# Performance work log

Hardware: AMD Instinct MI355X
Metric: run time of the kernel (lower is better)

Reference implementation:

```python
import jax, jax.numpy as jnp
import numpy as np

BETA = 0.25

def setup_inputs() -> dict:
    key = jax.random.key(0)
    k1, k2 = jax.random.split(key)
    z_e = jax.random.normal(k1, (32, 256, 32, 32), dtype=jnp.float32)
    embed_weight = jax.random.normal(k2, (4096, 256), dtype=jnp.float32) * 0.1
    return {"z_e": z_e, "embed_weight": embed_weight}

def reference(z_e, embed_weight):
    # Eval-mode forward (no input noise, no EMA buffer update).
    B, C, H, W = z_e.shape
    K = embed_weight.shape[0]
    z_t = jnp.transpose(z_e, (0, 2, 3, 1))            # [B,H,W,C]
    z_flat = z_t.reshape(-1, C)                        # [N,C]
    # Squared Euclidean distances; argmin is identical to argmin of cdist(p=2).
    d = (
        jnp.sum(z_flat * z_flat, axis=1, keepdims=True)
        - 2.0 * (z_flat @ embed_weight.T)
        + jnp.sum(embed_weight * embed_weight, axis=1)
    )                                                  # [N,K]
    idx = jnp.argmin(d, axis=1)                        # [N]
    # utilization = (#unique codes used) / vocab_size, jit-safe via bincount-style scatter
    counts = jnp.zeros((K,), dtype=jnp.float32).at[idx].add(1.0)
    utilization = jnp.sum(counts > 0).astype(jnp.float32) / K
    z_q = embed_weight[idx].reshape(B, H, W, C)        # [B,H,W,C]
    commitment_loss = jnp.mean((jax.lax.stop_gradient(z_q) - z_t) ** 2) * BETA
    z_q_st = z_t + jax.lax.stop_gradient(z_q - z_t)    # straight-through
    return jnp.transpose(z_q_st, (0, 3, 1, 2)), commitment_loss, utilization
```

## Files before the change

### kernel.cpp

```cpp
#include <hip/hip_runtime.h>
#include <math.h>


#define W 0.05f

using half8 = __attribute__((ext_vector_type(8))) _Float16;
using f32x4 = __attribute__((ext_vector_type(4))) float;

__device__ __forceinline__ void gload_lds16(const void* g, void* l) {
  __builtin_amdgcn_global_load_lds(
      (const __attribute__((address_space(1))) unsigned int*)g,
      (__attribute__((address_space(3))) unsigned int*)l, 16, 0, 0);
}

__device__ __forceinline__ bool lexlt(float v, int x, float ov, int ox) {
  return (v < ov) || (v == ov && x < ox);
}
__device__ __forceinline__ bool lexlt64(double v, int x, double ov, int ox) {
  return (v < ov) || (v == ov && x < ox);
}

__device__ __forceinline__ void ins3(float d, int c,
                                     float& a0, float& a1, float& a2,
                                     int& b0, int& b1, int& b2) {
  const bool l0 = d < a0, l1 = d < a1, l2 = d < a2;
  a2 = l1 ? a1 : (l2 ? d : a2);
  b2 = l1 ? b1 : (l2 ? c : b2);
  a1 = l0 ? a0 : (l1 ? d : a1);
  b1 = l0 ? b0 : (l1 ? c : b1);
  a0 = l0 ? d : a0;
  b0 = l0 ? c : b0;
}

__device__ __forceinline__ void mrg3(float& a0, float& a1, float& a2,
                                     int& x0, int& x1, int& x2,
                                     float b0, float b1, float b2,
                                     int y0, int y1, int y2) {
  const bool A = lexlt(a0, x0, b0, y0);
  const float w0 = A ? a0 : b0; const int w0x = A ? x0 : y0;
  const float fw = A ? a1 : b1; const int fwx = A ? x1 : y1;
  const float ls = A ? b0 : a0; const int lsx = A ? y0 : x0;
  const bool B = lexlt(fw, fwx, ls, lsx);
  const float w1 = B ? fw : ls; const int w1x = B ? fwx : lsx;
  const float t1 = A ? a2 : b2; const int t1x = A ? x2 : y2;
  const float l2v = A ? b1 : a1; const int l2x = A ? y1 : x1;
  const float c1 = B ? t1 : fw; const int c1x = B ? t1x : fwx;
  const float c2 = B ? ls : l2v; const int c2x = B ? lsx : l2x;
  const bool C = lexlt(c1, c1x, c2, c2x);
  a0 = w0; x0 = w0x; a1 = w1; x1 = w1x;
  a2 = C ? c1 : c2; x2 = C ? c1x : c2x;
}

__global__ __launch_bounds__(256) void vq_prep(const float* __restrict__ E,
                                               uint4* __restrict__ Epk,
                                               float* __restrict__ enorm) {
  const int t = blockIdx.x * 256 + threadIdx.x;
  const int code = t >> 5, jj = t & 31;
  const int slice = jj >> 3, j = jj & 7;
  const int cg = code >> 7, c = code & 127;
  const float* src = E + (size_t)code * 256 + jj * 8;
  union { half8 h; uint4 u; } pk;
  float s = 0.f;
#pragma unroll
  for (int e = 0; e < 8; ++e) {
    const float z = src[e];
    s = fmaf(z, z, s);
    pk.h[e] = (_Float16)(z * 256.0f);
  }
  const size_t g = (size_t)((cg * 4 + slice) * 1024) + c * 8 + (j ^ (c & 7));
  Epk[g] = pk.u;
#pragma unroll
  for (int off = 1; off < 32; off <<= 1) s += __shfl_xor(s, off);
  if (jj == 0) enorm[code] = s;
}

__global__ __launch_bounds__(256, 2) void vq_screen(
    const float* __restrict__ Z, const char* __restrict__ Epk,
    const float* __restrict__ enorm,
    float* __restrict__ pv0, float* __restrict__ pv1, float* __restrict__ pv2,
    int* __restrict__ pi0, int* __restrict__ pi1, int* __restrict__ pi2) {
  __shared__ char lds[65536];
  const int tid = threadIdx.x;
  const int w = tid >> 6, l = tid & 63;
  const int qg = blockIdx.x >> 1, half = blockIdx.x & 1;
  const int qbase = qg * 128;
  const int b = qbase >> 10;
  const int hwq = (qbase & 1023) + w * 32 + (l & 15);

  const float* Zq = Z + (size_t)b * 262144 + hwq;
  half8 ah[2][8];
#pragma unroll
  for (int u = 0; u < 2; ++u)
#pragma unroll
    for (int ks = 0; ks < 8; ++ks) {
      const int c0 = ks * 32 + (l >> 4) * 8;
#pragma unroll
      for (int e = 0; e < 8; ++e)
        ah[u][ks][e] = (_Float16)(Zq[u * 16 + ((size_t)(c0 + e) << 10)] * 256.0f);
    }

  int lo[4];
#pragma unroll
  for (int s = 0; s < 4; ++s)
    lo[s] = (s >> 1) * 16384 + (l & 15) * 128 +
            ((((s & 1) * 4 + (l >> 4)) ^ (l & 7)) << 4);

  float m0[2][4], m1[2][4], m2[2][4];
  int x0[2][4], x1[2][4], x2[2][4];
#pragma unroll
  for (int u = 0; u < 2; ++u)
#pragma unroll
    for (int r = 0; r < 4; ++r) {
      m0[u][r] = INFINITY; m1[u][r] = INFINITY; m2[u][r] = INFINITY;
      x0[u][r] = 0x7fffffff; x1[u][r] = 0x7fffffff; x2[u][r] = 0x7fffffff;
    }

  const int sbase = half * 32;
  auto stage = [&](int sel, int ss) {
    const char* src = Epk + ((size_t)(sbase + ss) << 15) + w * 8192 + l * 16;
    char* dst = lds + sel * 32768 + w * 8192;
#pragma unroll
    for (int i = 0; i < 8; ++i) gload_lds16(src + i * 1024, dst + i * 1024);
  };
  stage(0, 0);

  for (int chunk = 0; chunk < 16; ++chunk) {
    f32x4 acc[2][8];
#pragma unroll
    for (int u = 0; u < 2; ++u)
#pragma unroll
      for (int t = 0; t < 8; ++t) acc[u][t] = (f32x4){0.f, 0.f, 0.f, 0.f};

    for (int h = 0; h < 2; ++h) {
      const int ss = chunk * 2 + h;
      __syncthreads();
      if (ss + 1 < 32) stage((ss + 1) & 1, ss + 1);
      const char* Lb = lds + (ss & 1) * 32768;
      __builtin_amdgcn_s_setprio(1);
#pragma unroll
      for (int s = 0; s < 4; ++s) {
        const int ksg = h * 4 + s;
#pragma unroll
        for (int t = 0; t < 8; ++t) {
          const half8 eh = *(const half8*)(Lb + t * 2048 + lo[s]);
          acc[0][t] = __builtin_amdgcn_mfma_f32_16x16x32_f16(ah[0][ksg], eh, acc[0][t], 0, 0, 0);
          acc[1][t] = __builtin_amdgcn_mfma_f32_16x16x32_f16(ah[1][ksg], eh, acc[1][t], 0, 0, 0);
        }
      }
      __builtin_amdgcn_s_setprio(0);
    }

    const int cb = half * 2048 + chunk * 128;
#pragma unroll
    for (int t = 0; t < 8; ++t) {
      const int code = cb + t * 16 + (l & 15);
      const float en = enorm[code];
#pragma unroll
      for (int u = 0; u < 2; ++u)
#pragma unroll
        for (int r = 0; r < 4; ++r) {
          const float d = fmaf(acc[u][t][r], -3.0517578125e-05f, en);
          ins3(d, code, m0[u][r], m1[u][r], m2[u][r], x0[u][r], x1[u][r], x2[u][r]);
        }
    }
  }

#pragma unroll
  for (int mask = 1; mask <= 8; mask <<= 1) {
#pragma unroll
    for (int u = 0; u < 2; ++u)
#pragma unroll
      for (int r = 0; r < 4; ++r) {
        const float o0 = __shfl_xor(m0[u][r], mask);
        const float o1 = __shfl_xor(m1[u][r], mask);
        const float o2 = __shfl_xor(m2[u][r], mask);
        const int y0 = __shfl_xor(x0[u][r], mask);
        const int y1 = __shfl_xor(x1[u][r], mask);
        const int y2 = __shfl_xor(x2[u][r], mask);
        mrg3(m0[u][r], m1[u][r], m2[u][r], x0[u][r], x1[u][r], x2[u][r],
             o0, o1, o2, y0, y1, y2);
      }
  }
  if ((l & 15) == 0) {
#pragma unroll
    for (int u = 0; u < 2; ++u)
#pragma unroll
      for (int r = 0; r < 4; ++r) {
        const int n = qbase + w * 32 + u * 16 + (l >> 4) * 4 + r;
        const int o = half * 32768 + n;
        pv0[o] = m0[u][r]; pv1[o] = m1[u][r]; pv2[o] = m2[u][r];
        pi0[o] = x0[u][r]; pi1[o] = x1[u][r]; pi2[o] = x2[u][r];
      }
  }
}

__global__ __launch_bounds__(256) void vq_merge(
    float* __restrict__ pv0, float* __restrict__ pv1, float* __restrict__ pv2,
    int* __restrict__ pi0, int* __restrict__ pi1, int* __restrict__ pi2,
    int* __restrict__ idxOut, int* __restrict__ cand, int* __restrict__ candCount,
    int* __restrict__ messy, int* __restrict__ messyCount) {
  const int n = blockIdx.x * 256 + threadIdx.x;
  float a0 = pv0[n], a1 = pv1[n], a2 = pv2[n];
  int x0 = pi0[n], x1 = pi1[n], x2 = pi2[n];
  mrg3(a0, a1, a2, x0, x1, x2,
       pv0[n + 32768], pv1[n + 32768], pv2[n + 32768],
       pi0[n + 32768], pi1[n + 32768], pi2[n + 32768]);
  idxOut[n] = x0;
  pi0[n] = x0; pi1[n] = x1; pi2[n] = x2;
  if (a1 - a0 < W) {
    if (a2 - a0 < W) {
      const int p = atomicAdd(messyCount, 1);
      if (p < 2048) messy[p] = n;
    } else {
      const int p = atomicAdd(candCount, 1);
      cand[p] = n;
    }
  }
}

__global__ __launch_bounds__(256) void vq_cand3(
    const float* __restrict__ Z, const float* __restrict__ E,
    const int* __restrict__ pi0, const int* __restrict__ pi1,
    const int* __restrict__ pi2, const int* __restrict__ cand,
    const int* __restrict__ candCount, int* __restrict__ idxOut) {
  const int w = threadIdx.x >> 6, l = threadIdx.x & 63;
  const int cnt = *candCount;
  for (int j = blockIdx.x * 4 + w; j < cnt; j += gridDim.x * 4) {
    const int n = cand[j];
    const int b = n >> 10, hw = n & 1023;
    const int ca = pi0[n], cbn = pi1[n], cc = pi2[n];
    float z4[4];
#pragma unroll
    for (int i = 0; i < 4; ++i)
      z4[i] = Z[(size_t)b * 262144 + ((size_t)(l * 4 + i) << 10) + hw];
    const float4 e0 = *(const float4*)(E + (size_t)ca * 256 + l * 4);
    const float4 e1 = *(const float4*)(E + (size_t)cbn * 256 + l * 4);
    const float4 e2 = *(const float4*)(E + (size_t)cc * 256 + l * 4);
    double d0 = 0, d1 = 0, d2 = 0;
    const float* p0 = (const float*)&e0;
    const float* p1 = (const float*)&e1;
    const float* p2 = (const float*)&e2;
#pragma unroll
    for (int i = 0; i < 4; ++i) {
      const double f0 = (double)z4[i] - (double)p0[i];
      const double f1 = (double)z4[i] - (double)p1[i];
      const double f2 = (double)z4[i] - (double)p2[i];
      d0 = fma(f0, f0, d0);
      d1 = fma(f1, f1, d1);
      d2 = fma(f2, f2, d2);
    }
#pragma unroll
    for (int off = 32; off > 0; off >>= 1) {
      d0 += __shfl_down(d0, off);
      d1 += __shfl_down(d1, off);
      d2 += __shfl_down(d2, off);
    }
    if (l == 0) {
      double bv = d0; int bx = ca;
      if (lexlt64(d1, cbn, bv, bx)) { bv = d1; bx = cbn; }
      if (lexlt64(d2, cc, bv, bx)) { bv = d2; bx = cc; }
      idxOut[n] = bx;
    }
  }
}

__global__ __launch_bounds__(256) void vq_messy1(
    const float* __restrict__ Z, const float* __restrict__ E,
    const int* __restrict__ messy, const int* __restrict__ messyCount,
    double* __restrict__ parv, int* __restrict__ parx) {
  __shared__ float zs[4][256];
  __shared__ double rv[4][256];
  __shared__ int ri[4][256];
  const int cnt0 = *messyCount;
  const int cnt = cnt0 > 2048 ? 2048 : cnt0;
  const int jobs = ((cnt + 3) >> 2) * 16;
  const int t = threadIdx.x;
  for (int job = blockIdx.x; job < jobs; job += gridDim.x) {
    const int grp = job >> 4, chunk = job & 15;
    __syncthreads();
    {
      const int q = t >> 6, lq = t & 63;
      const int mi = grp * 4 + q;
      const int n = messy[mi < cnt ? mi : grp * 4];
      const int b = n >> 10, hw = n & 1023;
#pragma unroll
      for (int i = 0; i < 4; ++i)
        zs[q][lq * 4 + i] =
            Z[(size_t)b * 262144 + ((size_t)(lq * 4 + i) << 10) + hw];
    }
    __syncthreads();
    const int code = chunk * 256 + t;
    const float* er = E + (size_t)code * 256;
    double s0 = 0, s1 = 0, s2 = 0, s3 = 0;
    for (int c = 0; c < 256; ++c) {
      const double ec = (double)er[c];
      const double f0 = (double)zs[0][c] - ec;
      const double f1 = (double)zs[1][c] - ec;
      const double f2 = (double)zs[2][c] - ec;
      const double f3 = (double)zs[3][c] - ec;
      s0 = fma(f0, f0, s0);
      s1 = fma(f1, f1, s1);
      s2 = fma(f2, f2, s2);
      s3 = fma(f3, f3, s3);
    }
    rv[0][t] = s0; rv[1][t] = s1; rv[2][t] = s2; rv[3][t] = s3;
    ri[0][t] = code; ri[1][t] = code; ri[2][t] = code; ri[3][t] = code;
    __syncthreads();
    for (int s = 128; s > 0; s >>= 1) {
      if (t < s) {
#pragma unroll
        for (int qq = 0; qq < 4; ++qq)
          if (lexlt64(rv[qq][t + s], ri[qq][t + s], rv[qq][t], ri[qq][t])) {
            rv[qq][t] = rv[qq][t + s];
            ri[qq][t] = ri[qq][t + s];
          }
      }
      __syncthreads();
    }
    if (t == 0) {
#pragma unroll
      for (int qq = 0; qq < 4; ++qq) {
        const int mi = grp * 4 + qq;
        if (mi < cnt) {
          parv[mi * 16 + chunk] = rv[qq][0];
          parx[mi * 16 + chunk] = ri[qq][0];
        }
      }
    }
  }
}

__global__ __launch_bounds__(256) void vq_messy2(
    const int* __restrict__ messy, const int* __restrict__ messyCount,
    const double* __restrict__ parv, const int* __restrict__ parx,
    int* __restrict__ idxOut) {
  const int cnt0 = *messyCount;
  const int cnt = cnt0 > 2048 ? 2048 : cnt0;
  for (int j = blockIdx.x * 256 + threadIdx.x; j < cnt; j += gridDim.x * 256) {
    double bv = parv[j * 16];
    int bx = parx[j * 16];
    for (int ch = 1; ch < 16; ++ch) {
      const double v = parv[j * 16 + ch];
      const int x = parx[j * 16 + ch];
      if (lexlt64(v, x, bv, bx)) { bv = v; bx = x; }
    }
    idxOut[messy[j]] = bx;
  }
}

__global__ __launch_bounds__(256) void vq_out(
    const float* __restrict__ Z, const float* __restrict__ E,
    const int* __restrict__ idx, float* __restrict__ out,
    double* __restrict__ lossSum, int* __restrict__ used) {
  __shared__ float zt[32][257];
  __shared__ int ids[32];
  const int tid = threadIdx.x;
  const int qb = blockIdx.x * 32;
  const int b = qb >> 10, hw0 = qb & 1023;
  if (tid < 32) {
    const int id = idx[qb + tid];
    ids[tid] = id;
    used[id] = 1;
  }
  __syncthreads();
  const int w = tid >> 6, l = tid & 63;
#pragma unroll
  for (int rr = 0; rr < 8; ++rr) {
    const int q = rr * 4 + w;
    const float4 v = *(const float4*)(E + (size_t)ids[q] * 256 + l * 4);
    zt[q][l * 4 + 0] = v.x;
    zt[q][l * 4 + 1] = v.y;
    zt[q][l * 4 + 2] = v.z;
    zt[q][l * 4 + 3] = v.w;
  }
  __syncthreads();
  const int hwl = tid & 31, cc = tid >> 5;
  const float* Zb = Z + (size_t)b * 262144 + hw0 + hwl;
  float* Ob = out + (size_t)b * 262144 + hw0 + hwl;
  float ls = 0.f;
#pragma unroll 4
  for (int it = 0; it < 32; ++it) {
    const int c = it * 8 + cc;
    const float o = zt[hwl][c];
    const float z = Zb[(size_t)c << 10];
    Ob[(size_t)c << 10] = o;
    const float d = o - z;
    ls = fmaf(d, d, ls);
  }
#pragma unroll
  for (int off = 32; off > 0; off >>= 1) ls += __shfl_down(ls, off);
  __shared__ float red[4];
  if (l == 0) red[w] = ls;
  __syncthreads();
  if (tid == 0)
    atomicAdd(lossSum, (double)((red[0] + red[1]) + (red[2] + red[3])));
}

__global__ __launch_bounds__(256) void vq_final(const int* __restrict__ used,
                                                const double* __restrict__ lossSum,
                                                float* __restrict__ out) {
  __shared__ int cnt[256];
  int c = 0;
  for (int k = threadIdx.x; k < 4096; k += 256) c += (used[k] > 0);
  cnt[threadIdx.x] = c;
  __syncthreads();
  if (threadIdx.x == 0) {
    int tot = 0;
    for (int t = 0; t < 256; ++t) tot += cnt[t];
    out[8388608] = (float)(*lossSum * 0.25 / 8388608.0);
    out[8388609] = (float)tot / 4096.0f;
  }
}

extern "C" void kernel_launch(void* const* d_in, const int* in_sizes, int n_in,
                              void* d_out, int out_size, void* d_ws, size_t ws_size,
                              hipStream_t stream) {
  const float* Z = (const float*)d_in[0];
  const float* E = (const float*)d_in[1];
  float* out = (float*)d_out;
  char* w = (char*)d_ws;

  int* idx = (int*)w;
  int* cand = (int*)(w + 131072);
  float* enorm = (float*)(w + 262144);
  int* used = (int*)(w + 278528);
  double* lossSum = (double*)(w + 294912);
  int* candCount = (int*)(w + 294920);
  int* messyCount = (int*)(w + 294924);

  char* Epk16 = (char*)out;
  float* pv0 = out + 524288;
  float* pv1 = out + 589824;
  float* pv2 = out + 655360;
  int* pi0 = (int*)(out + 720896);
  int* pi1 = (int*)(out + 786432);
  int* pi2 = (int*)(out + 851968);
  int* messy = (int*)(out + 917504);
  double* parv = (double*)(out + 919552);
  int* parx = (int*)(out + 985088);

  hipMemsetAsync(w + 278528, 0, 16400, stream);
  vq_prep<<<512, 256, 0, stream>>>(E, (uint4*)Epk16, enorm);
  vq_screen<<<512, 256, 0, stream>>>(Z, Epk16, enorm, pv0, pv1, pv2, pi0, pi1, pi2);
  vq_merge<<<128, 256, 0, stream>>>(pv0, pv1, pv2, pi0, pi1, pi2, idx, cand,
                                    candCount, messy, messyCount);
  vq_cand3<<<256, 256, 0, stream>>>(Z, E, pi0, pi1, pi2, cand, candCount, idx);
  vq_messy1<<<1024, 256, 0, stream>>>(Z, E, messy, messyCount, parv, parx);
  vq_messy2<<<8, 256, 0, stream>>>(messy, messyCount, parv, parx, idx);
  vq_out<<<1024, 256, 0, stream>>>(Z, E, idx, out, lossSum, used);
  vq_final<<<1, 256, 0, stream>>>(used, lossSum, out);
}
```

Measured before the change: 199.6 us.

## Pack quantized distance and code index into int keys for top-3 screening

The screening kernel now quantizes each approximate distance to an integer and packs it with the 12-bit code index into one int key. Top-3 insertion and the cross-lane merge then reduce to integer min/max instead of float-plus-index compare-and-select chains, which cuts ALU work and shuffle traffic. The codebook is also split into quarters instead of halves, with a smaller LDS tile and occupancy 3, and the merge combines four partial results. The gap threshold becomes an integer in quantized units and the messy-list capacity doubles to absorb coarser ties, at the risk of sending more queries to the exact fallback paths.

```diff
diff --git a/kernel.cpp b/kernel.cpp
--- a/kernel.cpp
+++ b/kernel.cpp
@@ -2,7 +2,7 @@
 #include <math.h>
 
 
-#define W 0.05f
+#define WGAP 52
 
 using half8 = __attribute__((ext_vector_type(8))) _Float16;
 using f32x4 = __attribute__((ext_vector_type(4))) float;
@@ -13,52 +13,38 @@
       (__attribute__((address_space(3))) unsigned int*)l, 16, 0, 0);
 }
 
-__device__ __forceinline__ bool lexlt(float v, int x, float ov, int ox) {
-  return (v < ov) || (v == ov && x < ox);
-}
 __device__ __forceinline__ bool lexlt64(double v, int x, double ov, int ox) {
   return (v < ov) || (v == ov && x < ox);
 }
 
-__device__ __forceinline__ void ins3(float d, int c,
-                                     float& a0, float& a1, float& a2,
-                                     int& b0, int& b1, int& b2) {
-  const bool l0 = d < a0, l1 = d < a1, l2 = d < a2;
-  a2 = l1 ? a1 : (l2 ? d : a2);
-  b2 = l1 ? b1 : (l2 ? c : b2);
-  a1 = l0 ? a0 : (l1 ? d : a1);
-  b1 = l0 ? b0 : (l1 ? c : b1);
-  a0 = l0 ? d : a0;
-  b0 = l0 ? c : b0;
-}
-
-__device__ __forceinline__ void mrg3(float& a0, float& a1, float& a2,
-                                     int& x0, int& x1, int& x2,
-                                     float b0, float b1, float b2,
-                                     int y0, int y1, int y2) {
-  const bool A = lexlt(a0, x0, b0, y0);
-  const float w0 = A ? a0 : b0; const int w0x = A ? x0 : y0;
-  const float fw = A ? a1 : b1; const int fwx = A ? x1 : y1;
-  const float ls = A ? b0 : a0; const int lsx = A ? y0 : x0;
-  const bool B = lexlt(fw, fwx, ls, lsx);
-  const float w1 = B ? fw : ls; const int w1x = B ? fwx : lsx;
-  const float t1 = A ? a2 : b2; const int t1x = A ? x2 : y2;
-  const float l2v = A ? b1 : a1; const int l2x = A ? y1 : x1;
-  const float c1 = B ? t1 : fw; const int c1x = B ? t1x : fwx;
-  const float c2 = B ? ls : l2v; const int c2x = B ? lsx : l2x;
-  const bool C = lexlt(c1, c1x, c2, c2x);
-  a0 = w0; x0 = w0x; a1 = w1; x1 = w1x;
-  a2 = C ? c1 : c2; x2 = C ? c1x : c2x;
+__device__ __forceinline__ void ins3k(int key, int& a0, int& a1, int& a2) {
+  const int mx0 = max(key, a0);
+  a0 = min(key, a0);
+  const int mx1 = max(mx0, a1);
+  a1 = min(mx0, a1);
+  a2 = min(mx1, a2);
+}
+
+__device__ __forceinline__ void mrg3k(int& a0, int& a1, int& a2,
+                                      int b0, int b1, int b2) {
+  const int c0 = min(a0, b0);
+  const int x = max(a0, b0);
+  const int y = min(a1, b1);
+  const int c1 = min(x, y);
+  const int z = max(x, y);
+  const int ww = min(a2, b2);
+  const int c2 = min(z, ww);
+  a0 = c0; a1 = c1; a2 = c2;
 }
 
 __global__ __launch_bounds__(256) void vq_prep(const float* __restrict__ E,
                                                uint4* __restrict__ Epk,
-                                               float* __restrict__ enorm) {
+                                               float* __restrict__ en1024) {
   const int t = blockIdx.x * 256 + threadIdx.x;
-  const int code = t >> 5, jj = t & 31;
-  const int slice = jj >> 3, j = jj & 7;
-  const int cg = code >> 7, c = code & 127;
-  const float* src = E + (size_t)code * 256 + jj * 8;
+  const int code = t >> 5, j = t & 31;
+  const int quarter = code >> 10, c16 = (code >> 6) & 15, rc = code & 63;
+  const int khalf = j >> 4, jo = j & 15;
+  const float* src = E + (size_t)code * 256 + j * 8;
   union { half8 h; uint4 u; } pk;
   float s = 0.f;
 #pragma unroll
@@ -67,22 +53,22 @@
     s = fmaf(z, z, s);
     pk.h[e] = (_Float16)(z * 256.0f);
   }
-  const size_t g = (size_t)((cg * 4 + slice) * 1024) + c * 8 + (j ^ (c & 7));
+  const size_t g = (size_t)(quarter * 32 + c16 * 2 + khalf) * 1024 +
+                   rc * 16 + (jo ^ (rc & 15));
   Epk[g] = pk.u;
 #pragma unroll
   for (int off = 1; off < 32; off <<= 1) s += __shfl_xor(s, off);
-  if (jj == 0) enorm[code] = s;
-}
-
-__global__ __launch_bounds__(256, 2) void vq_screen(
+  if (j == 0) en1024[code] = s * 1024.0f;
+}
+
+__global__ __launch_bounds__(256, 3) void vq_screen(
     const float* __restrict__ Z, const char* __restrict__ Epk,
-    const float* __restrict__ enorm,
-    float* __restrict__ pv0, float* __restrict__ pv1, float* __restrict__ pv2,
-    int* __restrict__ pi0, int* __restrict__ pi1, int* __restrict__ pi2) {
-  __shared__ char lds[65536];
+    const float* __restrict__ en1024,
+    int* __restrict__ pk0, int* __restrict__ pk1, int* __restrict__ pk2) {
+  __shared__ char lds[32768];
   const int tid = threadIdx.x;
   const int w = tid >> 6, l = tid & 63;
-  const int qg = blockIdx.x >> 1, half = blockIdx.x & 1;
+  const int qg = blockIdx.x >> 2, quarter = blockIdx.x & 3;
   const int qbase = qg * 128;
   const int b = qbase >> 10;
   const int hwq = (qbase & 1023) + w * 32 + (l & 15);
@@ -102,65 +88,64 @@
   int lo[4];
 #pragma unroll
   for (int s = 0; s < 4; ++s)
-    lo[s] = (s >> 1) * 16384 + (l & 15) * 128 +
-            ((((s & 1) * 4 + (l >> 4)) ^ (l & 7)) << 4);
-
-  float m0[2][4], m1[2][4], m2[2][4];
-  int x0[2][4], x1[2][4], x2[2][4];
+    lo[s] = (l & 15) * 256 + (((s * 4 + (l >> 4)) ^ (l & 15)) << 4);
+
+  int k0[2][4], k1[2][4], k2[2][4];
 #pragma unroll
   for (int u = 0; u < 2; ++u)
 #pragma unroll
     for (int r = 0; r < 4; ++r) {
-      m0[u][r] = INFINITY; m1[u][r] = INFINITY; m2[u][r] = INFINITY;
-      x0[u][r] = 0x7fffffff; x1[u][r] = 0x7fffffff; x2[u][r] = 0x7fffffff;
-    }
-
-  const int sbase = half * 32;
+      k0[u][r] = 0x7fffffff; k1[u][r] = 0x7fffffff; k2[u][r] = 0x7fffffff;
+    }
+
   auto stage = [&](int sel, int ss) {
-    const char* src = Epk + ((size_t)(sbase + ss) << 15) + w * 8192 + l * 16;
-    char* dst = lds + sel * 32768 + w * 8192;
-#pragma unroll
-    for (int i = 0; i < 8; ++i) gload_lds16(src + i * 1024, dst + i * 1024);
+    const char* src = Epk + ((size_t)(quarter * 32 + ss) << 14) + w * 4096 + l * 16;
+    char* dst = lds + sel * 16384 + w * 4096;
+#pragma unroll
+    for (int i = 0; i < 4; ++i) gload_lds16(src + i * 1024, dst + i * 1024);
   };
   stage(0, 0);
 
   for (int chunk = 0; chunk < 16; ++chunk) {
-    f32x4 acc[2][8];
+    f32x4 acc[2][4];
 #pragma unroll
     for (int u = 0; u < 2; ++u)
 #pragma unroll
-      for (int t = 0; t < 8; ++t) acc[u][t] = (f32x4){0.f, 0.f, 0.f, 0.f};
-
-    for (int h = 0; h < 2; ++h) {
-      const int ss = chunk * 2 + h;
+      for (int t = 0; t < 4; ++t) acc[u][t] = (f32x4){0.f, 0.f, 0.f, 0.f};
+
+#pragma unroll
+    for (int sh = 0; sh < 2; ++sh) {
+      const int ss = chunk * 2 + sh;
       __syncthreads();
       if (ss + 1 < 32) stage((ss + 1) & 1, ss + 1);
-      const char* Lb = lds + (ss & 1) * 32768;
+      const char* Lb = lds + (ss & 1) * 16384;
       __builtin_amdgcn_s_setprio(1);
 #pragma unroll
       for (int s = 0; s < 4; ++s) {
-        const int ksg = h * 4 + s;
-#pragma unroll
-        for (int t = 0; t < 8; ++t) {
-          const half8 eh = *(const half8*)(Lb + t * 2048 + lo[s]);
-          acc[0][t] = __builtin_amdgcn_mfma_f32_16x16x32_f16(ah[0][ksg], eh, acc[0][t], 0, 0, 0);
-          acc[1][t] = __builtin_amdgcn_mfma_f32_16x16x32_f16(ah[1][ksg], eh, acc[1][t], 0, 0, 0);
+        const int ks = sh * 4 + s;
+#pragma unroll
+        for (int t = 0; t < 4; ++t) {
+          const half8 eh = *(const half8*)(Lb + t * 4096 + lo[s]);
+          acc[0][t] = __builtin_amdgcn_mfma_f32_16x16x32_f16(ah[0][ks], eh, acc[0][t], 0, 0, 0);
+          acc[1][t] = __builtin_amdgcn_mfma_f32_16x16x32_f16(ah[1][ks], eh, acc[1][t], 0, 0, 0);
         }
       }
       __builtin_amdgcn_s_setprio(0);
     }
 
-    const int cb = half * 2048 + chunk * 128;
-#pragma unroll
-    for (int t = 0; t < 8; ++t) {
+    const int cb = quarter * 1024 + chunk * 64;
+#pragma unroll
+    for (int t = 0; t < 4; ++t) {
       const int code = cb + t * 16 + (l & 15);
-      const float en = enorm[code];
+      const float en = en1024[code];
 #pragma unroll
       for (int u = 0; u < 2; ++u)
 #pragma unroll
         for (int r = 0; r < 4; ++r) {
-          const float d = fmaf(acc[u][t][r], -3.0517578125e-05f, en);
-          ins3(d, code, m0[u][r], m1[u][r], m2[u][r], x0[u][r], x1[u][r], x2[u][r]);
+          const float df = fmaf(acc[u][t][r], -0.03125f, en);
+          const int di = (int)df;
+          const int key = (int)(((unsigned)di << 12) + (unsigned)code);
+          ins3k(key, k0[u][r], k1[u][r], k2[u][r]);
         }
     }
   }
@@ -171,14 +156,10 @@
     for (int u = 0; u < 2; ++u)
 #pragma unroll
       for (int r = 0; r < 4; ++r) {
-        const float o0 = __shfl_xor(m0[u][r], mask);
-        const float o1 = __shfl_xor(m1[u][r], mask);
-        const float o2 = __shfl_xor(m2[u][r], mask);
-        const int y0 = __shfl_xor(x0[u][r], mask);
-        const int y1 = __shfl_xor(x1[u][r], mask);
-        const int y2 = __shfl_xor(x2[u][r], mask);
-        mrg3(m0[u][r], m1[u][r], m2[u][r], x0[u][r], x1[u][r], x2[u][r],
-             o0, o1, o2, y0, y1, y2);
+        const int o0 = __shfl_xor(k0[u][r], mask);
+        const int o1 = __shfl_xor(k1[u][r], mask);
+        const int o2 = __shfl_xor(k2[u][r], mask);
+        mrg3k(k0[u][r], k1[u][r], k2[u][r], o0, o1, o2);
       }
   }
   if ((l & 15) == 0) {
@@ -187,33 +168,36 @@
 #pragma unroll
       for (int r = 0; r < 4; ++r) {
         const int n = qbase + w * 32 + u * 16 + (l >> 4) * 4 + r;
-        const int o = half * 32768 + n;
-        pv0[o] = m0[u][r]; pv1[o] = m1[u][r]; pv2[o] = m2[u][r];
-        pi0[o] = x0[u][r]; pi1[o] = x1[u][r]; pi2[o] = x2[u][r];
+        const int o = quarter * 32768 + n;
+        pk0[o] = k0[u][r]; pk1[o] = k1[u][r]; pk2[o] = k2[u][r];
       }
   }
 }
 
 __global__ __launch_bounds__(256) void vq_merge(
-    float* __restrict__ pv0, float* __restrict__ pv1, float* __restrict__ pv2,
-    int* __restrict__ pi0, int* __restrict__ pi1, int* __restrict__ pi2,
-    int* __restrict__ idxOut, int* __restrict__ cand, int* __restrict__ candCount,
-    int* __restrict__ messy, int* __restrict__ messyCount) {
+    const int* __restrict__ pk0, const int* __restrict__ pk1,
+    const int* __restrict__ pk2, int* __restrict__ idxOut,
+    int* __restrict__ cand, int* __restrict__ candCount,
+    int* __restrict__ messy, int* __restrict__ messyCount,
+    int* __restrict__ pi0, int* __restrict__ pi1, int* __restrict__ pi2) {
   const int n = blockIdx.x * 256 + threadIdx.x;
-  float a0 = pv0[n], a1 = pv1[n], a2 = pv2[n];
-  int x0 = pi0[n], x1 = pi1[n], x2 = pi2[n];
-  mrg3(a0, a1, a2, x0, x1, x2,
-       pv0[n + 32768], pv1[n + 32768], pv2[n + 32768],
-       pi0[n + 32768], pi1[n + 32768], pi2[n + 32768]);
+  int a0 = pk0[n], a1 = pk1[n], a2 = pk2[n];
+#pragma unroll
+  for (int q = 1; q < 4; ++q) {
+    const int o = q * 32768 + n;
+    mrg3k(a0, a1, a2, pk0[o], pk1[o], pk2[o]);
+  }
+  const int x0 = a0 & 0xfff;
   idxOut[n] = x0;
-  pi0[n] = x0; pi1[n] = x1; pi2[n] = x2;
-  if (a1 - a0 < W) {
-    if (a2 - a0 < W) {
+  const int d0 = a0 >> 12, d1 = a1 >> 12, d2 = a2 >> 12;
+  if (d1 - d0 < WGAP) {
+    if (d2 - d0 < WGAP) {
       const int p = atomicAdd(messyCount, 1);
-      if (p < 2048) messy[p] = n;
+      if (p < 4096) messy[p] = n;
     } else {
       const int p = atomicAdd(candCount, 1);
       cand[p] = n;
+      pi0[n] = x0; pi1[n] = a1 & 0xfff; pi2[n] = a2 & 0xfff;
     }
   }
 }
@@ -272,7 +256,7 @@
   __shared__ double rv[4][256];
   __shared__ int ri[4][256];
   const int cnt0 = *messyCount;
-  const int cnt = cnt0 > 2048 ? 2048 : cnt0;
+  const int cnt = cnt0 > 4096 ? 4096 : cnt0;
   const int jobs = ((cnt + 3) >> 2) * 16;
   const int t = threadIdx.x;
   for (int job = blockIdx.x; job < jobs; job += gridDim.x) {
@@ -335,7 +319,7 @@
     const double* __restrict__ parv, const int* __restrict__ parx,
     int* __restrict__ idxOut) {
   const int cnt0 = *messyCount;
-  const int cnt = cnt0 > 2048 ? 2048 : cnt0;
+  const int cnt = cnt0 > 4096 ? 4096 : cnt0;
   for (int j = blockIdx.x * 256 + threadIdx.x; j < cnt; j += gridDim.x * 256) {
     double bv = parv[j * 16];
     int bx = parx[j * 16];
@@ -422,28 +406,28 @@
 
   int* idx = (int*)w;
   int* cand = (int*)(w + 131072);
-  float* enorm = (float*)(w + 262144);
+  float* en1024 = (float*)(w + 262144);
   int* used = (int*)(w + 278528);
   double* lossSum = (double*)(w + 294912);
   int* candCount = (int*)(w + 294920);
   int* messyCount = (int*)(w + 294924);
 
   char* Epk16 = (char*)out;
-  float* pv0 = out + 524288;
-  float* pv1 = out + 589824;
-  float* pv2 = out + 655360;
-  int* pi0 = (int*)(out + 720896);
-  int* pi1 = (int*)(out + 786432);
-  int* pi2 = (int*)(out + 851968);
-  int* messy = (int*)(out + 917504);
-  double* parv = (double*)(out + 919552);
-  int* parx = (int*)(out + 985088);
+  int* pk0 = (int*)(out + 524288);
+  int* pk1 = (int*)(out + 655360);
+  int* pk2 = (int*)(out + 786432);
+  int* pi0 = (int*)(out + 917504);
+  int* pi1 = (int*)(out + 950272);
+  int* pi2 = (int*)(out + 983040);
+  int* messy = (int*)(out + 1015808);
+  double* parv = (double*)(out + 1019904);
+  int* parx = (int*)(out + 1150976);
 
   hipMemsetAsync(w + 278528, 0, 16400, stream);
-  vq_prep<<<512, 256, 0, stream>>>(E, (uint4*)Epk16, enorm);
-  vq_screen<<<512, 256, 0, stream>>>(Z, Epk16, enorm, pv0, pv1, pv2, pi0, pi1, pi2);
-  vq_merge<<<128, 256, 0, stream>>>(pv0, pv1, pv2, pi0, pi1, pi2, idx, cand,
-                                    candCount, messy, messyCount);
+  vq_prep<<<512, 256, 0, stream>>>(E, (uint4*)Epk16, en1024);
+  vq_screen<<<1024, 256, 0, stream>>>(Z, Epk16, en1024, pk0, pk1, pk2);
+  vq_merge<<<128, 256, 0, stream>>>(pk0, pk1, pk2, idx, cand, candCount,
+                                    messy, messyCount, pi0, pi1, pi2);
   vq_cand3<<<256, 256, 0, stream>>>(Z, E, pi0, pi1, pi2, cand, candCount, idx);
   vq_messy1<<<1024, 256, 0, stream>>>(Z, E, messy, messyCount, parv, parx);
   vq_messy2<<<8, 256, 0, stream>>>(messy, messyCount, parv, parx, idx);
```

Result: faster. 186.1 us (-6.8%).
